# Performance work log

Hardware: AMD Instinct MI355X
Metric: run time of the kernel (lower is better)

Reference implementation:

```python
import jax, jax.numpy as jnp
import numpy as np

B, S, D = 4, 2048, 1024

def setup_inputs() -> dict:
    key = jax.random.key(0)
    kv, kk, kq, kw = jax.random.split(key, 4)
    scale = 1.0 / np.sqrt(D)
    v = jax.random.normal(kv, (B, S, D), dtype=jnp.float32)
    k = jax.random.normal(kk, (B, S, D), dtype=jnp.float32)
    q = jax.random.normal(kq, (B, S, D), dtype=jnp.float32)
    wi = jax.random.normal(kw, (D, D), dtype=jnp.float32) * scale
    mask = jnp.tril(jnp.ones((S, S), dtype=bool))[None, :, :]  # causal [1,S,S]
    return {"v": v, "k": k, "q": q, "wi": wi, "mask": mask}

def reference(v, k, q, wi, mask):
    # project q, k, v with the shared weight wi
    q = q @ wi
    k = k @ wi
    v = v @ wi
    # scaled dot-product scores [B,S,S]
    scores = jnp.einsum('bqd,bkd->bqk', q, k) / jnp.sqrt(jnp.asarray(q.shape[-1], q.dtype))
    scores = jnp.where(mask, scores, jnp.asarray(-1e10, scores.dtype))
    attn = jax.nn.softmax(scores, axis=-1)
    # residual: q + attn @ v
    return q + jnp.einsum('bqk,bkd->bqd', attn, v)
```

## Files before the change

kernel.cpp:

```cpp
#include <hip/hip_runtime.h>
#include <hip/hip_bf16.h>

typedef __hip_bfloat16 bf16;
typedef short bf16x8 __attribute__((ext_vector_type(8)));
typedef float f32x4 __attribute__((ext_vector_type(4)));

#define HT 16384

__device__ __forceinline__ void gload16(const void* g, void* l) {
    __builtin_amdgcn_global_load_lds(
        (const __attribute__((address_space(1))) void*)g,
        (__attribute__((address_space(3))) void*)l, 16, 0, 0);
}

__device__ __forceinline__ void stage_half(char* lds, const bf16* src, int ld,
                                           int rowbase, int k0, int slotIdx,
                                           int tid)
{
    char* dst = lds + (size_t)slotIdx * HT + tid * 16;
    const int sub = tid >> 3;
    const int cb  = ((tid & 7) ^ (sub & 7)) << 4;
    #pragma unroll
    for (int p = 0; p < 2; ++p) {
        const int row = p * 64 + sub;
        const char* g = (const char*)(src + (size_t)(rowbase + row) * ld + k0) + cb;
        gload16(g, dst + p * 8192);
    }
}

__device__ __forceinline__ bf16x8 ldsfrag(const char* lds, int slotIdx,
                                          int row, int ks, int cb0)
{
    return *(const bf16x8*)(lds + (size_t)slotIdx * HT
                            + row * 128 + (cb0 ^ (ks << 6)));
}

__device__ __forceinline__ float bf2f(short s) {
    union { float f; unsigned u; } c;
    c.u = ((unsigned)(unsigned short)s) << 16;
    return c.f;
}

__launch_bounds__(512, 2)
__global__ void proj_bn128(const bf16* __restrict__ A, const bf16* __restrict__ B,
                           bf16* __restrict__ C)
{
    extern __shared__ char lds[];
    const int orig = blockIdx.y * 8 + blockIdx.x;
    const int wk = (orig & 7) * 96 + (orig >> 3);
    const int bi = wk >> 3, bj = wk & 7;
    const int brow = bi * 256, bcol = bj * 128;

    const int tid  = threadIdx.x;
    const int lane = tid & 63;
    const int w    = tid >> 6;
    const int wm   = w >> 1, wn = w & 1;
    const int fr   = lane & 15, fq = lane >> 4;
    const int cb0  = ((fr & 7) ^ fq) << 4;
    const int slotA = wm >> 1;
    const int rA    = (wm & 1) * 64;
    const int rB    = wn * 64;
    const int NT    = 16;

    f32x4 acc[4][4] = {};
    bf16x8 af[4][2], bv[4][2];

    stage_half(lds, B, 1024, bcol,       0, 2, tid);
    stage_half(lds, A, 1024, brow,       0, 0, tid);
    stage_half(lds, A, 1024, brow + 128, 0, 1, tid);
    stage_half(lds, B, 1024, bcol,      64, 5, tid);
    asm volatile("s_waitcnt vmcnt(2)" ::: "memory");
    __builtin_amdgcn_s_barrier();

#define QUAD2(m0, n0)                                                         \
    _Pragma("unroll") for (int dm = 0; dm < 2; ++dm)                          \
    _Pragma("unroll") for (int dn = 0; dn < 2; ++dn)                          \
    _Pragma("unroll") for (int ks = 0; ks < 2; ++ks)                          \
        acc[(m0)+dm][(n0)+dn] = __builtin_amdgcn_mfma_f32_16x16x32_bf16(      \
            af[(m0)+dm][ks], bv[(n0)+dn][ks], acc[(m0)+dm][(n0)+dn], 0, 0, 0);

    for (int t = 0; t < NT; ++t) {
        const int buf = t & 1, nbuf = buf ^ 1;
        const int k1 = min(t + 1, NT - 1) << 6;
        const int k2 = min(t + 2, NT - 1) << 6;

        #pragma unroll
        for (int m = 0; m < 2; ++m)
            #pragma unroll
            for (int ks = 0; ks < 2; ++ks)
                af[m][ks] = ldsfrag(lds, buf * 3 + slotA, rA + m * 16 + fr, ks, cb0);
        #pragma unroll
        for (int n = 0; n < 2; ++n)
            #pragma unroll
            for (int ks = 0; ks < 2; ++ks)
                bv[n][ks] = ldsfrag(lds, buf * 3 + 2, rB + n * 16 + fr, ks, cb0);
        stage_half(lds, A, 1024, brow, k1, nbuf * 3 + 0, tid);
        __builtin_amdgcn_s_barrier();
        __builtin_amdgcn_s_setprio(1);
        QUAD2(0, 0)
        __builtin_amdgcn_s_setprio(0);
        __builtin_amdgcn_s_barrier();

        #pragma unroll
        for (int n = 2; n < 4; ++n)
            #pragma unroll
            for (int ks = 0; ks < 2; ++ks)
                bv[n][ks] = ldsfrag(lds, buf * 3 + 2, rB + n * 16 + fr, ks, cb0);
        stage_half(lds, A, 1024, brow + 128, k1, nbuf * 3 + 1, tid);
        __builtin_amdgcn_s_barrier();
        __builtin_amdgcn_s_setprio(1);
        QUAD2(0, 2)
        __builtin_amdgcn_s_setprio(0);
        __builtin_amdgcn_s_barrier();

        #pragma unroll
        for (int m = 2; m < 4; ++m)
            #pragma unroll
            for (int ks = 0; ks < 2; ++ks)
                af[m][ks] = ldsfrag(lds, buf * 3 + slotA, rA + m * 16 + fr, ks, cb0);
        stage_half(lds, B, 1024, bcol, k2, buf * 3 + 2, tid);
        __builtin_amdgcn_s_barrier();
        __builtin_amdgcn_s_setprio(1);
        QUAD2(2, 2)
        __builtin_amdgcn_s_setprio(0);
        __builtin_amdgcn_s_barrier();

        __builtin_amdgcn_s_setprio(1);
        QUAD2(2, 0)
        __builtin_amdgcn_s_setprio(0);
        asm volatile("s_waitcnt vmcnt(2)" ::: "memory");
        __builtin_amdgcn_s_barrier();
    }
#undef QUAD2

    #pragma unroll
    for (int mf = 0; mf < 4; ++mf) {
        const int r0 = brow + wm * 64 + mf * 16 + fq * 4;
        #pragma unroll
        for (int nf = 0; nf < 4; ++nf) {
            const int c = bcol + wn * 64 + nf * 16 + fr;
            #pragma unroll
            for (int j = 0; j < 4; ++j)
                C[(size_t)(r0 + j) * 1024 + c] = __float2bfloat16(acc[mf][nf][j]);
        }
    }
}

template<int MODE>
__device__ __forceinline__ void tile128(char* lds, const bf16* A, const bf16* B,
                                        bf16* Cb, float* Cf, const bf16* Res,
                                        int lda, int ldb, int ldcb,
                                        int brow, int bcol, int NT, float scale,
                                        int tid, int wm, int wn, int fr, int fq,
                                        int cb0)
{
    f32x4 acc[4][2] = {};
    bf16x8 af[4][2], bv[2][2];

    stage_half(lds, A, lda, brow, 0,  0, tid);
    stage_half(lds, B, ldb, bcol, 0,  3, tid);
    stage_half(lds, A, lda, brow, 64, 1, tid);
    stage_half(lds, B, ldb, bcol, 64, 4, tid);
    asm volatile("s_waitcnt vmcnt(4)" ::: "memory");
    __builtin_amdgcn_s_barrier();

    for (int t = 0; t < NT; ++t) {
        const int aslot = t % 3, bslot = 3 + (t & 1);
        const int k2 = min(t + 2, NT - 1) << 6;

        #pragma unroll
        for (int m = 0; m < 2; ++m)
            #pragma unroll
            for (int ks = 0; ks < 2; ++ks)
                af[m][ks] = ldsfrag(lds, aslot, wm * 64 + m * 16 + fr, ks, cb0);
        #pragma unroll
        for (int n = 0; n < 2; ++n)
            #pragma unroll
            for (int ks = 0; ks < 2; ++ks)
                bv[n][ks] = ldsfrag(lds, bslot, wn * 32 + n * 16 + fr, ks, cb0);
        stage_half(lds, A, lda, brow, k2, (t + 2) % 3, tid);
        __builtin_amdgcn_s_barrier();
        __builtin_amdgcn_s_setprio(1);
        #pragma unroll
        for (int m = 0; m < 2; ++m)
            #pragma unroll
            for (int n = 0; n < 2; ++n)
                #pragma unroll
                for (int ks = 0; ks < 2; ++ks)
                    acc[m][n] = __builtin_amdgcn_mfma_f32_16x16x32_bf16(
                        af[m][ks], bv[n][ks], acc[m][n], 0, 0, 0);
        __builtin_amdgcn_s_setprio(0);
        __builtin_amdgcn_s_barrier();

        #pragma unroll
        for (int m = 2; m < 4; ++m)
            #pragma unroll
            for (int ks = 0; ks < 2; ++ks)
                af[m][ks] = ldsfrag(lds, aslot, wm * 64 + m * 16 + fr, ks, cb0);
        stage_half(lds, B, ldb, bcol, k2, bslot, tid);
        __builtin_amdgcn_s_barrier();
        __builtin_amdgcn_s_setprio(1);
        #pragma unroll
        for (int m = 2; m < 4; ++m)
            #pragma unroll
            for (int n = 0; n < 2; ++n)
                #pragma unroll
                for (int ks = 0; ks < 2; ++ks)
                    acc[m][n] = __builtin_amdgcn_mfma_f32_16x16x32_bf16(
                        af[m][ks], bv[n][ks], acc[m][n], 0, 0, 0);
        __builtin_amdgcn_s_setprio(0);
        asm volatile("s_waitcnt vmcnt(4)" ::: "memory");
        __builtin_amdgcn_s_barrier();
    }

    #pragma unroll
    for (int mf = 0; mf < 4; ++mf) {
        const int r0 = brow + wm * 64 + mf * 16 + fq * 4;
        #pragma unroll
        for (int nf = 0; nf < 2; ++nf) {
            const int c = bcol + wn * 32 + nf * 16 + fr;
            #pragma unroll
            for (int j = 0; j < 4; ++j) {
                if (MODE == 1)
                    Cb[(size_t)(r0 + j) * ldcb + c] =
                        __float2bfloat16(acc[mf][nf][j] * scale);
                else
                    Cf[(size_t)(r0 + j) * ldcb + c] = acc[mf][nf][j] +
                        __bfloat162float(Res[(size_t)(r0 + j) * ldcb + c]);
            }
        }
    }
}

__launch_bounds__(512, 4)
__global__ void scores128(const bf16* __restrict__ qp, const bf16* __restrict__ kp,
                          bf16* __restrict__ P)
{
    extern __shared__ char lds[];
    const int j = blockIdx.x;
    int bi = (int)((__fsqrt_rn(8.0f * j + 1.0f) - 1.0f) * 0.5f);
    while ((bi + 1) * (bi + 2) / 2 <= j) ++bi;
    while (bi * (bi + 1) / 2 > j) --bi;
    const int bj = j - bi * (bi + 1) / 2;
    const int bz = blockIdx.z;

    const int tid  = threadIdx.x;
    const int lane = tid & 63;
    const int w    = tid >> 6;
    const int wm   = w >> 2, wn = w & 3;
    const int fr   = lane & 15, fq = lane >> 4;
    const int cb0  = ((fr & 7) ^ fq) << 4;

    tile128<1>(lds,
               qp + (size_t)bz * 2048 * 1024,
               kp + (size_t)bz * 2048 * 1024,
               P + (size_t)bz * 2048 * 2048, nullptr, nullptr,
               1024, 1024, 2048,
               bi * 128, bj * 128, 16, 0.03125f,
               tid, wm, wn, fr, fq, cb0);
}

__launch_bounds__(512, 4)
__global__ void pv128(const bf16* __restrict__ P, const bf16* __restrict__ V,
                      const bf16* __restrict__ R, float* __restrict__ C)
{
    extern __shared__ char lds[];
    const int pid = blockIdx.x, bj = blockIdx.y, bz = blockIdx.z;
    const bf16* Pb = P + (size_t)bz * 2048 * 2048;
    const bf16* Vb = V + (size_t)bz * 1024 * 2048;
    const bf16* Rb = R + (size_t)bz * 2048 * 1024;
    float* Cb = C + (size_t)bz * 2048 * 1024;

    const int tid  = threadIdx.x;
    const int lane = tid & 63;
    const int w    = tid >> 6;
    const int wm   = w >> 2, wn = w & 3;
    const int fr   = lane & 15, fq = lane >> 4;
    const int cb0  = ((fr & 7) ^ fq) << 4;
    const int bcol = bj * 128;

    tile128<2>(lds, Pb, Vb, nullptr, Cb, Rb, 2048, 2048, 1024,
               pid * 128, bcol, 2 * (pid + 1), 1.0f,
               tid, wm, wn, fr, fq, cb0);
    asm volatile("s_waitcnt vmcnt(0) lgkmcnt(0)" ::: "memory");
    __builtin_amdgcn_s_barrier();
    const int bi2 = 15 - pid;
    tile128<2>(lds, Pb, Vb, nullptr, Cb, Rb, 2048, 2048, 1024,
               bi2 * 128, bcol, 2 * (bi2 + 1), 1.0f,
               tid, wm, wn, fr, fq, cb0);
}

__global__ void convert_qkv(const float* __restrict__ q, const float* __restrict__ k,
                            const float* __restrict__ v, bf16* __restrict__ Xb)
{
    const int N8 = 8192 * 1024 / 8;
    const int total = 3 * N8;
    for (int i = blockIdx.x * 256 + threadIdx.x; i < total; i += gridDim.x * 256) {
        const int t = i / N8, j = i - t * N8;
        const float4* s = (t == 0) ? (const float4*)q
                        : (t == 1) ? (const float4*)k : (const float4*)v;
        float4 a = s[2 * j], bq = s[2 * j + 1];
        float vals[8] = {a.x, a.y, a.z, a.w, bq.x, bq.y, bq.z, bq.w};
        union { short h[8]; bf16x8 v8; } o;
        #pragma unroll
        for (int e = 0; e < 8; ++e) {
            bf16 hh = __float2bfloat16(vals[e]);
            o.h[e] = *(short*)&hh;
        }
        ((bf16x8*)Xb)[i] = o.v8;
    }
}

__global__ void transpose_wi(const float* __restrict__ wi, bf16* __restrict__ Wt)
{
    __shared__ float t[32][33];
    const int n0 = blockIdx.x * 32, k0 = blockIdx.y * 32;
    const int lx = threadIdx.x & 31, ly = threadIdx.x >> 5;
    for (int i = ly; i < 32; i += 8)
        t[i][lx] = wi[(size_t)(k0 + i) * 1024 + n0 + lx];
    __syncthreads();
    for (int i = ly; i < 32; i += 8)
        Wt[(size_t)(n0 + i) * 1024 + k0 + lx] = __float2bfloat16(t[lx][i]);
}

__global__ void transpose_vp(const bf16* __restrict__ vp, bf16* __restrict__ vpT)
{
    __shared__ bf16 t[32][33];
    const int b = blockIdx.z;
    const int d0 = blockIdx.x * 32, s0 = blockIdx.y * 32;
    const bf16* src = vp + (size_t)b * 2048 * 1024;
    bf16* dst = vpT + (size_t)b * 1024 * 2048;
    const int lx = threadIdx.x & 31, ly = threadIdx.x >> 5;
    for (int i = ly; i < 32; i += 8)
        t[i][lx] = src[(size_t)(s0 + i) * 1024 + d0 + lx];
    __syncthreads();
    for (int i = ly; i < 32; i += 8)
        dst[(size_t)(d0 + i) * 2048 + s0 + lx] = t[lx][i];
}

__launch_bounds__(256)
__global__ void softmax_rows(bf16* __restrict__ P)
{
    const int wid = threadIdx.x >> 6, lane = threadIdx.x & 63;
    const int r = blockIdx.x * 4 + wid, b = blockIdx.y;
    bf16* row = P + ((size_t)b * 2048 + r) * 2048;
    const int nv  = r + 1;
    const int rup = (r & ~255) + 256;

    float vals[4][8];
    float m = -1e30f;
    #pragma unroll
    for (int c = 0; c < 4; ++c) {
        const int k0 = c * 512 + lane * 8;
        if (k0 < rup) {
            bf16x8 x = *(const bf16x8*)(row + k0);
            #pragma unroll
            for (int j = 0; j < 8; ++j) {
                float f = (k0 + j < nv) ? bf2f(x[j]) : -1e30f;
                vals[c][j] = f;
                m = fmaxf(m, f);
            }
        } else {
            #pragma unroll
            for (int j = 0; j < 8; ++j) vals[c][j] = -1e30f;
        }
    }
    #pragma unroll
    for (int o = 32; o; o >>= 1) m = fmaxf(m, __shfl_xor(m, o));

    float sum = 0.f;
    #pragma unroll
    for (int c = 0; c < 4; ++c)
        #pragma unroll
        for (int j = 0; j < 8; ++j) {
            float e = __expf(vals[c][j] - m);
            vals[c][j] = e;
            sum += e;
        }
    #pragma unroll
    for (int o = 32; o; o >>= 1) sum += __shfl_xor(sum, o);
    const float inv = 1.0f / sum;

    #pragma unroll
    for (int c = 0; c < 4; ++c) {
        const int k0 = c * 512 + lane * 8;
        if (k0 < rup) {
            union { short h[8]; bf16x8 v8; } o;
            #pragma unroll
            for (int j = 0; j < 8; ++j) {
                bf16 hh = __float2bfloat16(vals[c][j] * inv);
                o.h[j] = *(short*)&hh;
            }
            *(bf16x8*)(row + k0) = o.v8;
        }
    }
}

extern "C" void kernel_launch(void* const* d_in, const int* in_sizes, int n_in,
                              void* d_out, int out_size, void* d_ws, size_t ws_size,
                              hipStream_t stream)
{
    const float* v  = (const float*)d_in[0];
    const float* k  = (const float*)d_in[1];
    const float* q  = (const float*)d_in[2];
    const float* wi = (const float*)d_in[3];
    float* out = (float*)d_out;

    char* ws = (char*)d_ws;
    const size_t WT_OFF   = 0;
    const size_t PROJ_OFF = WT_OFF + (2u << 20);
    const size_t VPT_OFF  = PROJ_OFF + (size_t)24576 * 1024 * 2;
    const size_t XB_OFF   = VPT_OFF + (size_t)4 * 1024 * 2048 * 2;

    bf16* Wt   = (bf16*)(ws + WT_OFF);
    bf16* proj = (bf16*)(ws + PROJ_OFF);
    bf16* vpT  = (bf16*)(ws + VPT_OFF);
    bf16* Xb   = (bf16*)(ws + XB_OFF);
    bf16* P    = Xb;

    bf16* qp_b = proj;
    bf16* kp_b = proj + (size_t)8192 * 1024;
    bf16* vp_b = proj + (size_t)16384 * 1024;

    (void)hipFuncSetAttribute((const void*)proj_bn128,
            hipFuncAttributeMaxDynamicSharedMemorySize, 98304);
    (void)hipFuncSetAttribute((const void*)scores128,
            hipFuncAttributeMaxDynamicSharedMemorySize, 81920);
    (void)hipFuncSetAttribute((const void*)pv128,
            hipFuncAttributeMaxDynamicSharedMemorySize, 81920);

    transpose_wi<<<dim3(32, 32), 256, 0, stream>>>(wi, Wt);
    convert_qkv<<<2048, 256, 0, stream>>>(q, k, v, Xb);

    proj_bn128<<<dim3(8, 96), 512, 98304, stream>>>(Xb, Wt, proj);

    transpose_vp<<<dim3(32, 64, 4), 256, 0, stream>>>(vp_b, vpT);

    scores128<<<dim3(136, 1, 4), 512, 81920, stream>>>(qp_b, kp_b, P);

    softmax_rows<<<dim3(512, 4), 256, 0, stream>>>(P);

    pv128<<<dim3(8, 8, 4), 512, 81920, stream>>>(P, vpT, qp_b, out);
}
```

Measured before the change: 183.7 us.

## Deepen projection GEMM pipeline, merge conversion kernels, tighten softmax read range

The projection GEMM moves from double buffering to triple buffering of the A and B LDS tiles, issuing prefetches two to three k-steps ahead with adjusted vmcnt waits. This is meant to hide more global-load latency, at the cost of more LDS per block. The wi transpose and the q/k/v fp32-to-bf16 conversion are merged into one launch, removing a kernel boundary. Softmax now rounds each row's read extent up to a 128 boundary instead of 256, skipping reads of fully masked columns.

Measured after the change: 180.6 us. No clear change (-1.7%).

```diff
diff --git a/kernel.cpp b/kernel.cpp
--- a/kernel.cpp
+++ b/kernel.cpp
@@ -42,13 +42,13 @@
 }
 
 __launch_bounds__(512, 2)
-__global__ void proj_bn128(const bf16* __restrict__ A, const bf16* __restrict__ B,
-                           bf16* __restrict__ C)
+__global__ void proj_deep(const bf16* __restrict__ A, const bf16* __restrict__ B,
+                          bf16* __restrict__ C)
 {
     extern __shared__ char lds[];
     const int orig = blockIdx.y * 8 + blockIdx.x;
-    const int wk = (orig & 7) * 96 + (orig >> 3);
-    const int bi = wk >> 3, bj = wk & 7;
+    const int wk2 = (orig & 7) * 96 + (orig >> 3);
+    const int bi = wk2 >> 3, bj = wk2 & 7;
     const int brow = bi * 256, bcol = bj * 128;
 
     const int tid  = threadIdx.x;
@@ -57,7 +57,7 @@
     const int wm   = w >> 1, wn = w & 1;
     const int fr   = lane & 15, fq = lane >> 4;
     const int cb0  = ((fr & 7) ^ fq) << 4;
-    const int slotA = wm >> 1;
+    const int hA    = wm >> 1;
     const int rA    = (wm & 1) * 64;
     const int rB    = wn * 64;
     const int NT    = 16;
@@ -65,11 +65,14 @@
     f32x4 acc[4][4] = {};
     bf16x8 af[4][2], bv[4][2];
 
-    stage_half(lds, B, 1024, bcol,       0, 2, tid);
     stage_half(lds, A, 1024, brow,       0, 0, tid);
     stage_half(lds, A, 1024, brow + 128, 0, 1, tid);
-    stage_half(lds, B, 1024, bcol,      64, 5, tid);
-    asm volatile("s_waitcnt vmcnt(2)" ::: "memory");
+    stage_half(lds, B, 1024, bcol,       0, 6, tid);
+    stage_half(lds, A, 1024, brow,      64, 2, tid);
+    stage_half(lds, A, 1024, brow + 128,64, 3, tid);
+    stage_half(lds, B, 1024, bcol,     64, 7, tid);
+    stage_half(lds, B, 1024, bcol,    128, 8, tid);
+    asm volatile("s_waitcnt vmcnt(8)" ::: "memory");
     __builtin_amdgcn_s_barrier();
 
 #define QUAD2(m0, n0)                                                         \
@@ -80,21 +83,24 @@
             af[(m0)+dm][ks], bv[(n0)+dn][ks], acc[(m0)+dm][(n0)+dn], 0, 0, 0);
 
     for (int t = 0; t < NT; ++t) {
-        const int buf = t & 1, nbuf = buf ^ 1;
-        const int k1 = min(t + 1, NT - 1) << 6;
-        const int k2 = min(t + 2, NT - 1) << 6;
+        const int ab  = t % 3;
+        const int bb  = 6 + ab;
+        const int ab2 = ((t + 2) % 3) * 2;
+        const int kA  = min(t + 2, NT - 1) << 6;
+        const int kB  = min(t + 3, NT - 1) << 6;
+        const int slotA = ab * 2 + hA;
 
         #pragma unroll
         for (int m = 0; m < 2; ++m)
             #pragma unroll
             for (int ks = 0; ks < 2; ++ks)
-                af[m][ks] = ldsfrag(lds, buf * 3 + slotA, rA + m * 16 + fr, ks, cb0);
+                af[m][ks] = ldsfrag(lds, slotA, rA + m * 16 + fr, ks, cb0);
         #pragma unroll
         for (int n = 0; n < 2; ++n)
             #pragma unroll
             for (int ks = 0; ks < 2; ++ks)
-                bv[n][ks] = ldsfrag(lds, buf * 3 + 2, rB + n * 16 + fr, ks, cb0);
-        stage_half(lds, A, 1024, brow, k1, nbuf * 3 + 0, tid);
+                bv[n][ks] = ldsfrag(lds, bb, rB + n * 16 + fr, ks, cb0);
+        stage_half(lds, A, 1024, brow, kA, ab2, tid);
         __builtin_amdgcn_s_barrier();
         __builtin_amdgcn_s_setprio(1);
         QUAD2(0, 0)
@@ -105,8 +111,8 @@
         for (int n = 2; n < 4; ++n)
             #pragma unroll
             for (int ks = 0; ks < 2; ++ks)
-                bv[n][ks] = ldsfrag(lds, buf * 3 + 2, rB + n * 16 + fr, ks, cb0);
-        stage_half(lds, A, 1024, brow + 128, k1, nbuf * 3 + 1, tid);
+                bv[n][ks] = ldsfrag(lds, bb, rB + n * 16 + fr, ks, cb0);
+        stage_half(lds, A, 1024, brow + 128, kA, ab2 + 1, tid);
         __builtin_amdgcn_s_barrier();
         __builtin_amdgcn_s_setprio(1);
         QUAD2(0, 2)
@@ -117,8 +123,8 @@
         for (int m = 2; m < 4; ++m)
             #pragma unroll
             for (int ks = 0; ks < 2; ++ks)
-                af[m][ks] = ldsfrag(lds, buf * 3 + slotA, rA + m * 16 + fr, ks, cb0);
-        stage_half(lds, B, 1024, bcol, k2, buf * 3 + 2, tid);
+                af[m][ks] = ldsfrag(lds, slotA, rA + m * 16 + fr, ks, cb0);
+        stage_half(lds, B, 1024, bcol, kB, bb, tid);
         __builtin_amdgcn_s_barrier();
         __builtin_amdgcn_s_setprio(1);
         QUAD2(2, 2)
@@ -128,7 +134,7 @@
         __builtin_amdgcn_s_setprio(1);
         QUAD2(2, 0)
         __builtin_amdgcn_s_setprio(0);
-        asm volatile("s_waitcnt vmcnt(2)" ::: "memory");
+        asm volatile("s_waitcnt vmcnt(6)" ::: "memory");
         __builtin_amdgcn_s_barrier();
     }
 #undef QUAD2
@@ -290,15 +296,31 @@
                tid, wm, wn, fr, fq, cb0);
 }
 
-__global__ void convert_qkv(const float* __restrict__ q, const float* __restrict__ k,
-                            const float* __restrict__ v, bf16* __restrict__ Xb)
-{
+__global__ void convert_and_wi(const float* __restrict__ q,
+                               const float* __restrict__ k,
+                               const float* __restrict__ v,
+                               const float* __restrict__ wi,
+                               bf16* __restrict__ Xb, bf16* __restrict__ Wt)
+{
+    __shared__ float t[32][33];
+    if (blockIdx.x < 1024) {
+        const int n0 = (blockIdx.x & 31) * 32, k0 = (blockIdx.x >> 5) * 32;
+        const int lx = threadIdx.x & 31, ly = threadIdx.x >> 5;
+        for (int i = ly; i < 32; i += 8)
+            t[i][lx] = wi[(size_t)(k0 + i) * 1024 + n0 + lx];
+        __syncthreads();
+        for (int i = ly; i < 32; i += 8)
+            Wt[(size_t)(n0 + i) * 1024 + k0 + lx] = __float2bfloat16(t[lx][i]);
+        return;
+    }
     const int N8 = 8192 * 1024 / 8;
     const int total = 3 * N8;
-    for (int i = blockIdx.x * 256 + threadIdx.x; i < total; i += gridDim.x * 256) {
-        const int t = i / N8, j = i - t * N8;
-        const float4* s = (t == 0) ? (const float4*)q
-                        : (t == 1) ? (const float4*)k : (const float4*)v;
+    const int nconv = gridDim.x - 1024;
+    for (int i = (blockIdx.x - 1024) * 256 + threadIdx.x; i < total;
+         i += nconv * 256) {
+        const int ti = i / N8, j = i - ti * N8;
+        const float4* s = (ti == 0) ? (const float4*)q
+                        : (ti == 1) ? (const float4*)k : (const float4*)v;
         float4 a = s[2 * j], bq = s[2 * j + 1];
         float vals[8] = {a.x, a.y, a.z, a.w, bq.x, bq.y, bq.z, bq.w};
         union { short h[8]; bf16x8 v8; } o;
@@ -309,18 +331,6 @@
         }
         ((bf16x8*)Xb)[i] = o.v8;
     }
-}
-
-__global__ void transpose_wi(const float* __restrict__ wi, bf16* __restrict__ Wt)
-{
-    __shared__ float t[32][33];
-    const int n0 = blockIdx.x * 32, k0 = blockIdx.y * 32;
-    const int lx = threadIdx.x & 31, ly = threadIdx.x >> 5;
-    for (int i = ly; i < 32; i += 8)
-        t[i][lx] = wi[(size_t)(k0 + i) * 1024 + n0 + lx];
-    __syncthreads();
-    for (int i = ly; i < 32; i += 8)
-        Wt[(size_t)(n0 + i) * 1024 + k0 + lx] = __float2bfloat16(t[lx][i]);
 }
 
 __global__ void transpose_vp(const bf16* __restrict__ vp, bf16* __restrict__ vpT)
@@ -345,7 +355,7 @@
     const int r = blockIdx.x * 4 + wid, b = blockIdx.y;
     bf16* row = P + ((size_t)b * 2048 + r) * 2048;
     const int nv  = r + 1;
-    const int rup = (r & ~255) + 256;
+    const int rup = (r & ~127) + 128;
 
     float vals[4][8];
     float m = -1e30f;
@@ -422,17 +432,16 @@
     bf16* kp_b = proj + (size_t)8192 * 1024;
     bf16* vp_b = proj + (size_t)16384 * 1024;
 
-    (void)hipFuncSetAttribute((const void*)proj_bn128,
-            hipFuncAttributeMaxDynamicSharedMemorySize, 98304);
+    (void)hipFuncSetAttribute((const void*)proj_deep,
+            hipFuncAttributeMaxDynamicSharedMemorySize, 147456);
     (void)hipFuncSetAttribute((const void*)scores128,
             hipFuncAttributeMaxDynamicSharedMemorySize, 81920);
     (void)hipFuncSetAttribute((const void*)pv128,
             hipFuncAttributeMaxDynamicSharedMemorySize, 81920);
 
-    transpose_wi<<<dim3(32, 32), 256, 0, stream>>>(wi, Wt);
-    convert_qkv<<<2048, 256, 0, stream>>>(q, k, v, Xb);
-
-    proj_bn128<<<dim3(8, 96), 512, 98304, stream>>>(Xb, Wt, proj);
+    convert_and_wi<<<3072, 256, 0, stream>>>(q, k, v, wi, Xb, Wt);
+
+    proj_deep<<<dim3(8, 96), 512, 147456, stream>>>(Xb, Wt, proj);
 
     transpose_vp<<<dim3(32, 64, 4), 256, 0, stream>>>(vp_b, vpT);
 
```
